# Optimization experiments

Measured on AMD Instinct MI355X. Metric: run time of the kernel, lower is better.

## Reference

```python
import jax, jax.numpy as jnp
import numpy as np

N, E = 20000, 5000
IN_FT, OUT_FT = 128, 128
DENSITY = 0.01  # fraction of nonzeros in the incidence matrix


def setup_inputs() -> dict:
    key = jax.random.key(0)
    kx, kh, kw, kb = jax.random.split(key, 4)
    X = jax.random.normal(kx, (N, IN_FT), dtype=jnp.float32)
    H = (jax.random.uniform(kh, (N, E)) < DENSITY).astype(jnp.float32)
    # xavier_normal_ with gain=0.01
    xav_std = 0.01 * np.sqrt(2.0 / (IN_FT + OUT_FT))
    weight_trans = jax.random.normal(kw, (IN_FT, OUT_FT), dtype=jnp.float32) * xav_std
    bias = jax.random.normal(kb, (OUT_FT,), dtype=jnp.float32) * 0.01
    return {"X": X, "H": H, "weight_trans": weight_trans, "bias": bias}


def reference(X, H, weight_trans, bias):
    # X: [N, in_ft], H: [N, E] incidence
    Xw = X @ weight_trans                      # [N, out_ft]
    DV = jnp.sum(H, axis=1) + 1e-12            # node degrees, [N]
    DE = jnp.sum(H, axis=0) + 1e-12            # hyperedge degrees, [E]
    # G = diag(1/DV) @ H @ diag(1/DE) @ H^T applied to Xw, computed in the
    # efficient order without materializing the NxN matrix G:
    M = H.T @ Xw                               # [E, out_ft]
    M = M / DE[:, None]                        # diag(1/DE) scaling
    out = H @ M                                # [N, out_ft]
    out = out / DV[:, None]                    # diag(1/DV) scaling
    out = out + bias
    return jax.nn.relu(out)
```

## Files before the change

### kernel.cpp

```cpp
#include <hip/hip_runtime.h>
#include <hip/hip_bf16.h>

typedef unsigned long long u64;
typedef unsigned int u32;
typedef unsigned short u16;
typedef __attribute__((ext_vector_type(4))) float f32x4v;
typedef __attribute__((ext_vector_type(16))) float f32x16;
typedef __attribute__((ext_vector_type(8))) short bf16x8;

#define N_NODES 20000
#define N_EDGES 5000
#define FT 128
#define NT 20
#define NRG 313
#define ROW_U64 80
#define COL_STRIDE 5120
#define XWT_S 20032

#define NTLOAD(p) __builtin_nontemporal_load((const f32x4v*)(p))

static __device__ __forceinline__ u64 spread4(u64 x) {
  x = (x | (x << 24)) & 0x000000FF000000FFull;
  x = (x | (x << 12)) & 0x000F000F000F000Full;
  x = (x | (x << 6))  & 0x0303030303030303ull;
  x = (x | (x << 3))  & 0x1111111111111111ull;
  return x;
}

static __device__ __forceinline__ u16 f2bf(float x) {
  u32 u = __float_as_uint(x);
  u = (u + 0x7FFFu + ((u >> 16) & 1u)) >> 16;
  return (u16)u;
}

static __device__ __forceinline__ bf16x8 expand8(u32 b) {
  union { u32 u[4]; bf16x8 v; } r;
  r.u[0] = (( b        & 1u) | ((( b >> 1) & 1u) << 16)) * 0x3F80u;
  r.u[1] = (((b >> 2)  & 1u) | ((( b >> 3) & 1u) << 16)) * 0x3F80u;
  r.u[2] = (((b >> 4)  & 1u) | ((( b >> 5) & 1u) << 16)) * 0x3F80u;
  r.u[3] = (((b >> 6)  & 1u) | ((( b >> 7) & 1u) << 16)) * 0x3F80u;
  return r.v;
}

static __device__ __forceinline__ int swz(int c, int r) {
  return c * 256 + (((r + c) & 31) << 3);
}

__global__ __launch_bounds__(256) void scan_fused(
    const float* __restrict__ H, u64* __restrict__ Hbt2, u64* __restrict__ HbtT,
    const float2* __restrict__ X2, __hip_bfloat162* __restrict__ Xb2,
    const float* __restrict__ Wf, u16* __restrict__ WtB) {
  const int wid = threadIdx.x >> 6, lane = threadIdx.x & 63;

  if (blockIdx.x >= 1565) {
    for (int i = (blockIdx.x - 1565) * 256 + threadIdx.x; i < 1280000;
         i += 320 * 256)
      Xb2[i] = __float22bfloat162_rn(X2[i]);
    if (blockIdx.x == 1884) {
      for (int i = threadIdx.x; i < FT * FT; i += 256) {
        int f = i >> 7, k = i & 127;
        WtB[i] = f2bf(Wf[k * FT + f]);
      }
    }
    return;
  }

  const int gw = blockIdx.x * 4 + wid;
  const int t = gw % NT, rg = gw / NT;
  const int r0 = rg * 64;
  const int rows = min(64, N_NODES - r0);
  const int idx4 = t * 64 + lane;
  const bool lv = idx4 < 1250;

  u64 m0 = 0, m1 = 0, m2 = 0, m3 = 0;
  for (int kb = 0; kb < rows; kb += 8) {
    f32x4v vv[8];
#pragma unroll
    for (int k = 0; k < 8; ++k) vv[k] = (f32x4v){0.f, 0.f, 0.f, 0.f};
    if (lv) {
      const float* bp = H + (size_t)(r0 + kb) * N_EDGES + idx4 * 4;
#pragma unroll
      for (int k = 0; k < 8; ++k) vv[k] = NTLOAD(bp + (size_t)k * N_EDGES);
    }
#pragma unroll
    for (int k = 0; k < 8; ++k) {
      u64 b0 = __ballot(vv[k].x != 0.f);
      u64 b1 = __ballot(vv[k].y != 0.f);
      u64 b2 = __ballot(vv[k].z != 0.f);
      u64 b3 = __ballot(vv[k].w != 0.f);
      const bool keep = (lane == kb + k);
      m0 = keep ? b0 : m0;  m1 = keep ? b1 : m1;
      m2 = keep ? b2 : m2;  m3 = keep ? b3 : m3;
    }
  }
  if (lane < rows) {
#pragma unroll
    for (int j = 0; j < 4; ++j) {
      u64 p = spread4((m0 >> (16 * j)) & 0xFFFFull)
            | (spread4((m1 >> (16 * j)) & 0xFFFFull) << 1)
            | (spread4((m2 >> (16 * j)) & 0xFFFFull) << 2)
            | (spread4((m3 >> (16 * j)) & 0xFFFFull) << 3);
      Hbt2[(size_t)(t * 4 + j) * N_NODES + (r0 + lane)] = p;
    }
  }
  u64 t0 = 0, t1 = 0, t2 = 0, t3 = 0;
  for (int l = 0; l < 64; ++l) {
    u64 c0 = __ballot((m0 >> l) & 1ull);
    u64 c1 = __ballot((m1 >> l) & 1ull);
    u64 c2 = __ballot((m2 >> l) & 1ull);
    u64 c3 = __ballot((m3 >> l) & 1ull);
    const bool keep = (lane == l);
    t0 = keep ? c0 : t0;  t1 = keep ? c1 : t1;
    t2 = keep ? c2 : t2;  t3 = keep ? c3 : t3;
  }
  u64* op = HbtT + (size_t)rg * COL_STRIDE + t * 256 + 4 * lane;
  op[0] = t0; op[1] = t1; op[2] = t2; op[3] = t3;
}

__global__ __launch_bounds__(256) void gemm_xw(
    const u16* __restrict__ Xb, const u16* __restrict__ WtB,
    u16* __restrict__ XwT) {
  __shared__ u16 xt[4096];
  const int wave = threadIdx.x >> 6, lane = threadIdx.x & 63;
  const int col = lane & 31, half = lane >> 5;
  const int n0 = blockIdx.x * 32;
  const int f0 = wave * 32;
  if (n0 >= N_NODES) {
    if (lane < 32)
      for (int r = 0; r < 32; ++r)
        XwT[(size_t)(f0 + r) * XWT_S + n0 + lane] = 0;
    return;
  }
  {
    const int sn = threadIdx.x >> 3, sc = threadIdx.x & 7;
#pragma unroll
    for (int j = 0; j < 2; ++j) {
      bf16x8 v = *(const bf16x8*)(Xb + (size_t)(n0 + sn) * FT + (sc + 8 * j) * 8);
      *(bf16x8*)(xt + sn * 128 + (((sc + 8 * j) + sn) & 15) * 8) = v;
    }
  }
  __syncthreads();
  f32x16 acc;
#pragma unroll
  for (int i = 0; i < 16; ++i) acc[i] = 0.f;
#pragma unroll
  for (int kc = 0; kc < 16; kc += 2) {
    int c = kc + half;
    bf16x8 a = *(const bf16x8*)(WtB + (f0 + col) * FT + c * 8);
    bf16x8 b = *(const bf16x8*)(xt + col * 128 + ((c + col) & 15) * 8);
    acc = __builtin_amdgcn_mfma_f32_32x32x16_bf16(a, b, acc, 0, 0, 0);
  }
#pragma unroll
  for (int r = 0; r < 16; ++r) {
    int fr = (r & 3) + 8 * (r >> 2) + 4 * half;
    XwT[(size_t)(f0 + fr) * XWT_S + n0 + col] = f2bf(acc[r]);
  }
}

__global__ __launch_bounds__(256) void edge_gemm(
    const u16* __restrict__ XwT, const u64* __restrict__ HbtT,
    u16* __restrict__ MhT) {
  __shared__ u16 atile[4][2][2048];
  __shared__ float sdv[4][32];
  const int tid = threadIdx.x;
  const int wid = tid >> 6, lane = tid & 63;
  const int col = lane & 31, half = lane >> 5;

  const int et = blockIdx.x % 160, ft = blockIdx.x / 160;
  const int e0 = et * 32, f0 = ft * 32;
  const int ws_ = wid * 78 + (wid > 0 ? 1 : 0);
  const int we_ = ws_ + (wid == 0 ? 79 : 78);

  const int srow = lane >> 3, schunk = lane & 7;
  const u16* sgbase = XwT + (size_t)(f0 + srow) * XWT_S + schunk * 8;
  u16* buf0 = &atile[wid][0][0];
  u16* buf1 = &atile[wid][1][0];

  f32x16 acc;
#pragma unroll
  for (int i = 0; i < 16; ++i) acc[i] = 0.f;
  float dv = 0.f;

  bf16x8 rB[4], rC[4];
  {
    const int w1 = (ws_ + 1 < we_) ? ws_ + 1 : ws_;
    bf16x8 rA[4];
#pragma unroll
    for (int j = 0; j < 4; ++j)
      rA[j] = *(const bf16x8*)(sgbase + (size_t)(8 * j) * XWT_S + ws_ * 64);
#pragma unroll
    for (int j = 0; j < 4; ++j)
      rB[j] = *(const bf16x8*)(sgbase + (size_t)(8 * j) * XWT_S + w1 * 64);
#pragma unroll
    for (int j = 0; j < 4; ++j)
      *(bf16x8*)(buf0 + swz(schunk, srow + 8 * j)) = rA[j];
  }
  u64 h0 = HbtT[(size_t)ws_ * COL_STRIDE + e0 + col];
  u64 h1 = HbtT[(size_t)((ws_ + 1 < we_) ? ws_ + 1 : ws_) * COL_STRIDE + e0 + col];

  int p = 0;
  for (int w = ws_; w < we_; ++w) {
    const int w2 = (w + 2 < we_) ? w + 2 : we_ - 1;
#pragma unroll
    for (int j = 0; j < 4; ++j)
      rC[j] = *(const bf16x8*)(sgbase + (size_t)(8 * j) * XWT_S + w2 * 64);
    u64 h2 = HbtT[(size_t)w2 * COL_STRIDE + e0 + col];

    const u16* ab = p ? buf1 : buf0;
#pragma unroll
    for (int q = 0; q < 4; ++q) {
      bf16x8 a = *(const bf16x8*)(ab + swz(2 * q + half, col));
      bf16x8 b = expand8((u32)(h0 >> (q * 16 + half * 8)) & 0xFFu);
      acc = __builtin_amdgcn_mfma_f32_32x32x16_bf16(a, b, acc, 0, 0, 0);
    }
    dv += (float)__popcll(h0);

    u16* nb = p ? buf0 : buf1;
#pragma unroll
    for (int j = 0; j < 4; ++j)
      *(bf16x8*)(nb + swz(schunk, srow + 8 * j)) = rB[j];
#pragma unroll
    for (int j = 0; j < 4; ++j) rB[j] = rC[j];
    h0 = h1; h1 = h2; p ^= 1;
  }

  float* sacc = (float*)&atile[wid][0][0];
#pragma unroll
  for (int r = 0; r < 16; ++r) {
    int fr = (r & 3) + 8 * (r >> 2) + 4 * half;
    sacc[fr * 32 + col] = acc[r];
  }
  if (half == 0) sdv[wid][col] = dv;
  __syncthreads();

  {
    const int frl = tid >> 3, eq = tid & 7;
    const float* s0 = (const float*)&atile[0][0][0];
    union { u16 h[4]; u64 q; } o;
#pragma unroll
    for (int j = 0; j < 4; ++j) {
      int e = eq * 4 + j;
      int idx = frl * 32 + e;
      float s = s0[idx] + s0[2048 + idx] + s0[4096 + idx] + s0[6144 + idx];
      float d = sdv[0][e] + sdv[1][e] + sdv[2][e] + sdv[3][e];
      o.h[j] = f2bf(s / (d + 1e-12f));
    }
    *(u64*)(MhT + (size_t)(f0 + frl) * COL_STRIDE + e0 + eq * 4) = o.q;
  }
}

__global__ __launch_bounds__(256) void node_gemm(
    const u64* __restrict__ Hbt2, const u16* __restrict__ MhT,
    const float* __restrict__ bias, float* __restrict__ out) {
  __shared__ u16 btile[4][2][2048];
  const int tid = threadIdx.x;
  const int wid = tid >> 6, lane = tid & 63;
  const int col = lane & 31, half = lane >> 5;
  const int n0 = blockIdx.x * 32;
  const int f0 = wid * 32;

  const int srow = lane >> 3, schunk = lane & 7;
  const u16* sgbase = MhT + (size_t)(f0 + srow) * COL_STRIDE + schunk * 8;
  u16* buf0 = &btile[wid][0][0];
  u16* buf1 = &btile[wid][1][0];

  f32x16 acc;
#pragma unroll
  for (int i = 0; i < 16; ++i) acc[i] = 0.f;
  float dv = 0.f;

  bf16x8 rB[4], rC[4];
  {
    bf16x8 rA[4];
#pragma unroll
    for (int j = 0; j < 4; ++j)
      rA[j] = *(const bf16x8*)(sgbase + (size_t)(8 * j) * COL_STRIDE);
#pragma unroll
    for (int j = 0; j < 4; ++j)
      rB[j] = *(const bf16x8*)(sgbase + (size_t)(8 * j) * COL_STRIDE + 64);
#pragma unroll
    for (int j = 0; j < 4; ++j)
      *(bf16x8*)(buf0 + swz(schunk, srow + 8 * j)) = rA[j];
  }
  u64 h0 = Hbt2[(size_t)0 * N_NODES + n0 + col];
  u64 h1 = Hbt2[(size_t)1 * N_NODES + n0 + col];

  int p = 0;
  for (int w = 0; w < ROW_U64; ++w) {
    const int w2 = (w + 2 < ROW_U64) ? w + 2 : ROW_U64 - 1;
#pragma unroll
    for (int j = 0; j < 4; ++j)
      rC[j] = *(const bf16x8*)(sgbase + (size_t)(8 * j) * COL_STRIDE + w2 * 64);
    u64 h2 = Hbt2[(size_t)w2 * N_NODES + n0 + col];

    const u16* bb = p ? buf1 : buf0;
#pragma unroll
    for (int q = 0; q < 4; ++q) {
      bf16x8 a = expand8((u32)(h0 >> (q * 16 + half * 8)) & 0xFFu);
      bf16x8 b = *(const bf16x8*)(bb + swz(2 * q + half, col));
      acc = __builtin_amdgcn_mfma_f32_32x32x16_bf16(a, b, acc, 0, 0, 0);
    }
    dv += (float)__popcll(h0);

    u16* nb = p ? buf0 : buf1;
#pragma unroll
    for (int j = 0; j < 4; ++j)
      *(bf16x8*)(nb + swz(schunk, srow + 8 * j)) = rB[j];
#pragma unroll
    for (int j = 0; j < 4; ++j) rB[j] = rC[j];
    h0 = h1; h1 = h2; p ^= 1;
  }

  float inv = 1.f / (dv + 1e-12f);
  float bb = bias[f0 + col];
#pragma unroll
  for (int r = 0; r < 16; ++r) {
    int rr = (r & 3) + 8 * (r >> 2) + 4 * half;
    float iv = __shfl(inv, rr);
    out[(size_t)(n0 + rr) * FT + f0 + col] = fmaxf(fmaf(acc[r], iv, bb), 0.f);
  }
}

extern "C" void kernel_launch(void* const* d_in, const int* in_sizes, int n_in,
                              void* d_out, int out_size, void* d_ws, size_t ws_size,
                              hipStream_t stream) {
  const float* X    = (const float*)d_in[0];
  const float* H    = (const float*)d_in[1];
  const float* W    = (const float*)d_in[2];
  const float* bias = (const float*)d_in[3];
  float* out = (float*)d_out;

  int* ws = (int*)d_ws;
  u64* Hbt2            = (u64*)ws;
  u64* HbtT            = (u64*)(ws + 3200000);
  __hip_bfloat162* Xb2 = (__hip_bfloat162*)(ws + 6405120);
  u16* MhT             = (u16*)(ws + 6405120);
  u16* WtB             = (u16*)(ws + 7685120);
  u16* XwT             = (u16*)(ws + 7693312);

  scan_fused<<<1885, 256, 0, stream>>>(H, Hbt2, HbtT, (const float2*)X, Xb2,
                                       W, WtB);
  gemm_xw   <<<626, 256, 0, stream>>>((const u16*)Xb2, WtB, XwT);
  edge_gemm <<<640, 256, 0, stream>>>(XwT, HbtT, MhT);
  node_gemm <<<625, 256, 0, stream>>>(Hbt2, MhT, bias, out);
}
```

Measured before the change: 653.5 us.

## Fuse four stage kernels into one persistent kernel with grid barriers

Merges the scan, Xw GEMM, edge GEMM and node GEMM kernels into a single persistent kernel of 768 blocks that loops over virtual block indices. Stages are separated by atomic-counter grid barriers, and shared memory is held in a union sized for the largest stage. The aim is to remove three kernel launches and the gaps between them. In exchange it adds a memset launch, spin-wait barriers that rely on every block being co-resident, and a fixed grid that may leave work unevenly spread across CUs within each stage.

```diff
diff --git a/kernel.cpp b/kernel.cpp
--- a/kernel.cpp
+++ b/kernel.cpp
@@ -16,6 +16,7 @@
 #define ROW_U64 80
 #define COL_STRIDE 5120
 #define XWT_S 20032
+#define GRID 768
 
 #define NTLOAD(p) __builtin_nontemporal_load((const f32x4v*)(p))
 
@@ -46,287 +47,303 @@
   return c * 256 + (((r + c) & 31) << 3);
 }
 
-__global__ __launch_bounds__(256) void scan_fused(
+static __device__ __forceinline__ void gbar(int* bar, int target) {
+  __syncthreads();
+  if (threadIdx.x == 0) {
+    __threadfence();
+    atomicAdd(bar, 1);
+    int spins = 0;
+    while (__hip_atomic_load(bar, __ATOMIC_RELAXED,
+                             __HIP_MEMORY_SCOPE_AGENT) < target) {
+      __builtin_amdgcn_s_sleep(4);
+      if (++spins > (1 << 26)) break;
+    }
+    __threadfence();
+  }
+  __syncthreads();
+}
+
+union SharedU {
+  struct { u16 xt[4096]; } x;
+  struct { u16 atile[4][2][2048]; float sdv[4][32]; } e;
+  struct { u16 btile[4][2][2048]; } n;
+};
+
+__global__ __launch_bounds__(256, 3) void mega(
     const float* __restrict__ H, u64* __restrict__ Hbt2, u64* __restrict__ HbtT,
     const float2* __restrict__ X2, __hip_bfloat162* __restrict__ Xb2,
-    const float* __restrict__ Wf, u16* __restrict__ WtB) {
-  const int wid = threadIdx.x >> 6, lane = threadIdx.x & 63;
-
-  if (blockIdx.x >= 1565) {
-    for (int i = (blockIdx.x - 1565) * 256 + threadIdx.x; i < 1280000;
-         i += 320 * 256)
-      Xb2[i] = __float22bfloat162_rn(X2[i]);
-    if (blockIdx.x == 1884) {
-      for (int i = threadIdx.x; i < FT * FT; i += 256) {
-        int f = i >> 7, k = i & 127;
-        WtB[i] = f2bf(Wf[k * FT + f]);
-      }
-    }
-    return;
-  }
-
-  const int gw = blockIdx.x * 4 + wid;
-  const int t = gw % NT, rg = gw / NT;
-  const int r0 = rg * 64;
-  const int rows = min(64, N_NODES - r0);
-  const int idx4 = t * 64 + lane;
-  const bool lv = idx4 < 1250;
-
-  u64 m0 = 0, m1 = 0, m2 = 0, m3 = 0;
-  for (int kb = 0; kb < rows; kb += 8) {
-    f32x4v vv[8];
-#pragma unroll
-    for (int k = 0; k < 8; ++k) vv[k] = (f32x4v){0.f, 0.f, 0.f, 0.f};
-    if (lv) {
-      const float* bp = H + (size_t)(r0 + kb) * N_EDGES + idx4 * 4;
-#pragma unroll
-      for (int k = 0; k < 8; ++k) vv[k] = NTLOAD(bp + (size_t)k * N_EDGES);
-    }
-#pragma unroll
-    for (int k = 0; k < 8; ++k) {
-      u64 b0 = __ballot(vv[k].x != 0.f);
-      u64 b1 = __ballot(vv[k].y != 0.f);
-      u64 b2 = __ballot(vv[k].z != 0.f);
-      u64 b3 = __ballot(vv[k].w != 0.f);
-      const bool keep = (lane == kb + k);
-      m0 = keep ? b0 : m0;  m1 = keep ? b1 : m1;
-      m2 = keep ? b2 : m2;  m3 = keep ? b3 : m3;
-    }
-  }
-  if (lane < rows) {
-#pragma unroll
-    for (int j = 0; j < 4; ++j) {
-      u64 p = spread4((m0 >> (16 * j)) & 0xFFFFull)
-            | (spread4((m1 >> (16 * j)) & 0xFFFFull) << 1)
-            | (spread4((m2 >> (16 * j)) & 0xFFFFull) << 2)
-            | (spread4((m3 >> (16 * j)) & 0xFFFFull) << 3);
-      Hbt2[(size_t)(t * 4 + j) * N_NODES + (r0 + lane)] = p;
-    }
-  }
-  u64 t0 = 0, t1 = 0, t2 = 0, t3 = 0;
-  for (int l = 0; l < 64; ++l) {
-    u64 c0 = __ballot((m0 >> l) & 1ull);
-    u64 c1 = __ballot((m1 >> l) & 1ull);
-    u64 c2 = __ballot((m2 >> l) & 1ull);
-    u64 c3 = __ballot((m3 >> l) & 1ull);
-    const bool keep = (lane == l);
-    t0 = keep ? c0 : t0;  t1 = keep ? c1 : t1;
-    t2 = keep ? c2 : t2;  t3 = keep ? c3 : t3;
-  }
-  u64* op = HbtT + (size_t)rg * COL_STRIDE + t * 256 + 4 * lane;
-  op[0] = t0; op[1] = t1; op[2] = t2; op[3] = t3;
-}
-
-__global__ __launch_bounds__(256) void gemm_xw(
-    const u16* __restrict__ Xb, const u16* __restrict__ WtB,
-    u16* __restrict__ XwT) {
-  __shared__ u16 xt[4096];
-  const int wave = threadIdx.x >> 6, lane = threadIdx.x & 63;
-  const int col = lane & 31, half = lane >> 5;
-  const int n0 = blockIdx.x * 32;
-  const int f0 = wave * 32;
-  if (n0 >= N_NODES) {
-    if (lane < 32)
-      for (int r = 0; r < 32; ++r)
-        XwT[(size_t)(f0 + r) * XWT_S + n0 + lane] = 0;
-    return;
-  }
-  {
-    const int sn = threadIdx.x >> 3, sc = threadIdx.x & 7;
-#pragma unroll
-    for (int j = 0; j < 2; ++j) {
-      bf16x8 v = *(const bf16x8*)(Xb + (size_t)(n0 + sn) * FT + (sc + 8 * j) * 8);
-      *(bf16x8*)(xt + sn * 128 + (((sc + 8 * j) + sn) & 15) * 8) = v;
-    }
-  }
-  __syncthreads();
-  f32x16 acc;
-#pragma unroll
-  for (int i = 0; i < 16; ++i) acc[i] = 0.f;
-#pragma unroll
-  for (int kc = 0; kc < 16; kc += 2) {
-    int c = kc + half;
-    bf16x8 a = *(const bf16x8*)(WtB + (f0 + col) * FT + c * 8);
-    bf16x8 b = *(const bf16x8*)(xt + col * 128 + ((c + col) & 15) * 8);
-    acc = __builtin_amdgcn_mfma_f32_32x32x16_bf16(a, b, acc, 0, 0, 0);
-  }
-#pragma unroll
-  for (int r = 0; r < 16; ++r) {
-    int fr = (r & 3) + 8 * (r >> 2) + 4 * half;
-    XwT[(size_t)(f0 + fr) * XWT_S + n0 + col] = f2bf(acc[r]);
-  }
-}
-
-__global__ __launch_bounds__(256) void edge_gemm(
-    const u16* __restrict__ XwT, const u64* __restrict__ HbtT,
-    u16* __restrict__ MhT) {
-  __shared__ u16 atile[4][2][2048];
-  __shared__ float sdv[4][32];
+    const float* __restrict__ Wf, u16* __restrict__ WtB,
+    u16* __restrict__ XwT, u16* __restrict__ MhT,
+    const float* __restrict__ bias, float* __restrict__ out,
+    int* __restrict__ bar) {
+  __shared__ SharedU sh;
   const int tid = threadIdx.x;
   const int wid = tid >> 6, lane = tid & 63;
   const int col = lane & 31, half = lane >> 5;
 
-  const int et = blockIdx.x % 160, ft = blockIdx.x / 160;
-  const int e0 = et * 32, f0 = ft * 32;
-  const int ws_ = wid * 78 + (wid > 0 ? 1 : 0);
-  const int we_ = ws_ + (wid == 0 ? 79 : 78);
-
-  const int srow = lane >> 3, schunk = lane & 7;
-  const u16* sgbase = XwT + (size_t)(f0 + srow) * XWT_S + schunk * 8;
-  u16* buf0 = &atile[wid][0][0];
-  u16* buf1 = &atile[wid][1][0];
-
-  f32x16 acc;
-#pragma unroll
-  for (int i = 0; i < 16; ++i) acc[i] = 0.f;
-  float dv = 0.f;
-
-  bf16x8 rB[4], rC[4];
-  {
-    const int w1 = (ws_ + 1 < we_) ? ws_ + 1 : ws_;
-    bf16x8 rA[4];
-#pragma unroll
-    for (int j = 0; j < 4; ++j)
-      rA[j] = *(const bf16x8*)(sgbase + (size_t)(8 * j) * XWT_S + ws_ * 64);
-#pragma unroll
-    for (int j = 0; j < 4; ++j)
-      rB[j] = *(const bf16x8*)(sgbase + (size_t)(8 * j) * XWT_S + w1 * 64);
-#pragma unroll
-    for (int j = 0; j < 4; ++j)
-      *(bf16x8*)(buf0 + swz(schunk, srow + 8 * j)) = rA[j];
-  }
-  u64 h0 = HbtT[(size_t)ws_ * COL_STRIDE + e0 + col];
-  u64 h1 = HbtT[(size_t)((ws_ + 1 < we_) ? ws_ + 1 : ws_) * COL_STRIDE + e0 + col];
-
-  int p = 0;
-  for (int w = ws_; w < we_; ++w) {
-    const int w2 = (w + 2 < we_) ? w + 2 : we_ - 1;
-#pragma unroll
-    for (int j = 0; j < 4; ++j)
-      rC[j] = *(const bf16x8*)(sgbase + (size_t)(8 * j) * XWT_S + w2 * 64);
-    u64 h2 = HbtT[(size_t)w2 * COL_STRIDE + e0 + col];
-
-    const u16* ab = p ? buf1 : buf0;
-#pragma unroll
-    for (int q = 0; q < 4; ++q) {
-      bf16x8 a = *(const bf16x8*)(ab + swz(2 * q + half, col));
-      bf16x8 b = expand8((u32)(h0 >> (q * 16 + half * 8)) & 0xFFu);
-      acc = __builtin_amdgcn_mfma_f32_32x32x16_bf16(a, b, acc, 0, 0, 0);
-    }
-    dv += (float)__popcll(h0);
-
-    u16* nb = p ? buf0 : buf1;
-#pragma unroll
-    for (int j = 0; j < 4; ++j)
-      *(bf16x8*)(nb + swz(schunk, srow + 8 * j)) = rB[j];
-#pragma unroll
-    for (int j = 0; j < 4; ++j) rB[j] = rC[j];
-    h0 = h1; h1 = h2; p ^= 1;
-  }
-
-  float* sacc = (float*)&atile[wid][0][0];
-#pragma unroll
-  for (int r = 0; r < 16; ++r) {
-    int fr = (r & 3) + 8 * (r >> 2) + 4 * half;
-    sacc[fr * 32 + col] = acc[r];
-  }
-  if (half == 0) sdv[wid][col] = dv;
-  __syncthreads();
-
-  {
-    const int frl = tid >> 3, eq = tid & 7;
-    const float* s0 = (const float*)&atile[0][0][0];
-    union { u16 h[4]; u64 q; } o;
-#pragma unroll
-    for (int j = 0; j < 4; ++j) {
-      int e = eq * 4 + j;
-      int idx = frl * 32 + e;
-      float s = s0[idx] + s0[2048 + idx] + s0[4096 + idx] + s0[6144 + idx];
-      float d = sdv[0][e] + sdv[1][e] + sdv[2][e] + sdv[3][e];
-      o.h[j] = f2bf(s / (d + 1e-12f));
-    }
-    *(u64*)(MhT + (size_t)(f0 + frl) * COL_STRIDE + e0 + eq * 4) = o.q;
-  }
-}
-
-__global__ __launch_bounds__(256) void node_gemm(
-    const u64* __restrict__ Hbt2, const u16* __restrict__ MhT,
-    const float* __restrict__ bias, float* __restrict__ out) {
-  __shared__ u16 btile[4][2][2048];
-  const int tid = threadIdx.x;
-  const int wid = tid >> 6, lane = tid & 63;
-  const int col = lane & 31, half = lane >> 5;
-  const int n0 = blockIdx.x * 32;
-  const int f0 = wid * 32;
-
-  const int srow = lane >> 3, schunk = lane & 7;
-  const u16* sgbase = MhT + (size_t)(f0 + srow) * COL_STRIDE + schunk * 8;
-  u16* buf0 = &btile[wid][0][0];
-  u16* buf1 = &btile[wid][1][0];
-
-  f32x16 acc;
-#pragma unroll
-  for (int i = 0; i < 16; ++i) acc[i] = 0.f;
-  float dv = 0.f;
-
-  bf16x8 rB[4], rC[4];
-  {
-    bf16x8 rA[4];
-#pragma unroll
-    for (int j = 0; j < 4; ++j)
-      rA[j] = *(const bf16x8*)(sgbase + (size_t)(8 * j) * COL_STRIDE);
-#pragma unroll
-    for (int j = 0; j < 4; ++j)
-      rB[j] = *(const bf16x8*)(sgbase + (size_t)(8 * j) * COL_STRIDE + 64);
-#pragma unroll
-    for (int j = 0; j < 4; ++j)
-      *(bf16x8*)(buf0 + swz(schunk, srow + 8 * j)) = rA[j];
-  }
-  u64 h0 = Hbt2[(size_t)0 * N_NODES + n0 + col];
-  u64 h1 = Hbt2[(size_t)1 * N_NODES + n0 + col];
-
-  int p = 0;
-  for (int w = 0; w < ROW_U64; ++w) {
-    const int w2 = (w + 2 < ROW_U64) ? w + 2 : ROW_U64 - 1;
-#pragma unroll
-    for (int j = 0; j < 4; ++j)
-      rC[j] = *(const bf16x8*)(sgbase + (size_t)(8 * j) * COL_STRIDE + w2 * 64);
-    u64 h2 = Hbt2[(size_t)w2 * N_NODES + n0 + col];
-
-    const u16* bb = p ? buf1 : buf0;
-#pragma unroll
-    for (int q = 0; q < 4; ++q) {
-      bf16x8 a = expand8((u32)(h0 >> (q * 16 + half * 8)) & 0xFFu);
-      bf16x8 b = *(const bf16x8*)(bb + swz(2 * q + half, col));
-      acc = __builtin_amdgcn_mfma_f32_32x32x16_bf16(a, b, acc, 0, 0, 0);
-    }
-    dv += (float)__popcll(h0);
-
-    u16* nb = p ? buf0 : buf1;
-#pragma unroll
-    for (int j = 0; j < 4; ++j)
-      *(bf16x8*)(nb + swz(schunk, srow + 8 * j)) = rB[j];
-#pragma unroll
-    for (int j = 0; j < 4; ++j) rB[j] = rC[j];
-    h0 = h1; h1 = h2; p ^= 1;
-  }
-
-  float inv = 1.f / (dv + 1e-12f);
-  float bb = bias[f0 + col];
-#pragma unroll
-  for (int r = 0; r < 16; ++r) {
-    int rr = (r & 3) + 8 * (r >> 2) + 4 * half;
-    float iv = __shfl(inv, rr);
-    out[(size_t)(n0 + rr) * FT + f0 + col] = fmaxf(fmaf(acc[r], iv, bb), 0.f);
+  for (int vb = blockIdx.x; vb < 1885; vb += GRID) {
+    if (vb >= 1565) {
+      for (int i = (vb - 1565) * 256 + tid; i < 1280000; i += 320 * 256)
+        Xb2[i] = __float22bfloat162_rn(X2[i]);
+      if (vb == 1884) {
+        for (int i = tid; i < FT * FT; i += 256) {
+          int f = i >> 7, k = i & 127;
+          WtB[i] = f2bf(Wf[k * FT + f]);
+        }
+      }
+      continue;
+    }
+    const int gw = vb * 4 + wid;
+    const int t = gw % NT, rg = gw / NT;
+    const int r0 = rg * 64;
+    const int rows = min(64, N_NODES - r0);
+    const int idx4 = t * 64 + lane;
+    const bool lv = idx4 < 1250;
+
+    u64 m0 = 0, m1 = 0, m2 = 0, m3 = 0;
+    for (int kb = 0; kb < rows; kb += 8) {
+      f32x4v vv[8];
+#pragma unroll
+      for (int k = 0; k < 8; ++k) vv[k] = (f32x4v){0.f, 0.f, 0.f, 0.f};
+      if (lv) {
+        const float* bp = H + (size_t)(r0 + kb) * N_EDGES + idx4 * 4;
+#pragma unroll
+        for (int k = 0; k < 8; ++k) vv[k] = NTLOAD(bp + (size_t)k * N_EDGES);
+      }
+#pragma unroll
+      for (int k = 0; k < 8; ++k) {
+        u64 b0 = __ballot(vv[k].x != 0.f);
+        u64 b1 = __ballot(vv[k].y != 0.f);
+        u64 b2 = __ballot(vv[k].z != 0.f);
+        u64 b3 = __ballot(vv[k].w != 0.f);
+        const bool keep = (lane == kb + k);
+        m0 = keep ? b0 : m0;  m1 = keep ? b1 : m1;
+        m2 = keep ? b2 : m2;  m3 = keep ? b3 : m3;
+      }
+    }
+    if (lane < rows) {
+#pragma unroll
+      for (int j = 0; j < 4; ++j) {
+        u64 p = spread4((m0 >> (16 * j)) & 0xFFFFull)
+              | (spread4((m1 >> (16 * j)) & 0xFFFFull) << 1)
+              | (spread4((m2 >> (16 * j)) & 0xFFFFull) << 2)
+              | (spread4((m3 >> (16 * j)) & 0xFFFFull) << 3);
+        Hbt2[(size_t)(t * 4 + j) * N_NODES + (r0 + lane)] = p;
+      }
+    }
+    u64 t0 = 0, t1 = 0, t2 = 0, t3 = 0;
+    for (int l = 0; l < 64; ++l) {
+      u64 c0 = __ballot((m0 >> l) & 1ull);
+      u64 c1 = __ballot((m1 >> l) & 1ull);
+      u64 c2 = __ballot((m2 >> l) & 1ull);
+      u64 c3 = __ballot((m3 >> l) & 1ull);
+      const bool keep = (lane == l);
+      t0 = keep ? c0 : t0;  t1 = keep ? c1 : t1;
+      t2 = keep ? c2 : t2;  t3 = keep ? c3 : t3;
+    }
+    u64* op = HbtT + (size_t)rg * COL_STRIDE + t * 256 + 4 * lane;
+    op[0] = t0; op[1] = t1; op[2] = t2; op[3] = t3;
+  }
+  gbar(bar, GRID);
+
+  for (int vb = blockIdx.x; vb < 626; vb += GRID) {
+    const int n0 = vb * 32;
+    const int f0 = wid * 32;
+    if (n0 >= N_NODES) {
+      if (lane < 32)
+        for (int r = 0; r < 32; ++r)
+          XwT[(size_t)(f0 + r) * XWT_S + n0 + lane] = 0;
+    } else {
+      __syncthreads();
+      const u16* Xb = (const u16*)Xb2;
+      {
+        const int sn = tid >> 3, sc = tid & 7;
+#pragma unroll
+        for (int j = 0; j < 2; ++j) {
+          bf16x8 v = *(const bf16x8*)(Xb + (size_t)(n0 + sn) * FT + (sc + 8 * j) * 8);
+          *(bf16x8*)(sh.x.xt + sn * 128 + (((sc + 8 * j) + sn) & 15) * 8) = v;
+        }
+      }
+      __syncthreads();
+      f32x16 acc;
+#pragma unroll
+      for (int i = 0; i < 16; ++i) acc[i] = 0.f;
+#pragma unroll
+      for (int kc = 0; kc < 16; kc += 2) {
+        int c = kc + half;
+        bf16x8 a = *(const bf16x8*)(WtB + (f0 + col) * FT + c * 8);
+        bf16x8 b = *(const bf16x8*)(sh.x.xt + col * 128 + ((c + col) & 15) * 8);
+        acc = __builtin_amdgcn_mfma_f32_32x32x16_bf16(a, b, acc, 0, 0, 0);
+      }
+#pragma unroll
+      for (int r = 0; r < 16; ++r) {
+        int fr = (r & 3) + 8 * (r >> 2) + 4 * half;
+        XwT[(size_t)(f0 + fr) * XWT_S + n0 + col] = f2bf(acc[r]);
+      }
+    }
+  }
+  gbar(bar, 2 * GRID);
+
+  for (int vb = blockIdx.x; vb < 640; vb += GRID) {
+    const int et = vb % 160, ft = vb / 160;
+    const int e0 = et * 32, f0 = ft * 32;
+    const int ws_ = wid * 78 + (wid > 0 ? 1 : 0);
+    const int we_ = ws_ + (wid == 0 ? 79 : 78);
+
+    const int srow = lane >> 3, schunk = lane & 7;
+    const u16* sgbase = XwT + (size_t)(f0 + srow) * XWT_S + schunk * 8;
+    u16* buf0 = &sh.e.atile[wid][0][0];
+    u16* buf1 = &sh.e.atile[wid][1][0];
+
+    __syncthreads();
+
+    f32x16 acc;
+#pragma unroll
+    for (int i = 0; i < 16; ++i) acc[i] = 0.f;
+    float dv = 0.f;
+
+    bf16x8 rB[4], rC[4];
+    {
+      const int w1 = (ws_ + 1 < we_) ? ws_ + 1 : ws_;
+      bf16x8 rA[4];
+#pragma unroll
+      for (int j = 0; j < 4; ++j)
+        rA[j] = *(const bf16x8*)(sgbase + (size_t)(8 * j) * XWT_S + ws_ * 64);
+#pragma unroll
+      for (int j = 0; j < 4; ++j)
+        rB[j] = *(const bf16x8*)(sgbase + (size_t)(8 * j) * XWT_S + w1 * 64);
+#pragma unroll
+      for (int j = 0; j < 4; ++j)
+        *(bf16x8*)(buf0 + swz(schunk, srow + 8 * j)) = rA[j];
+    }
+    u64 h0 = HbtT[(size_t)ws_ * COL_STRIDE + e0 + col];
+    u64 h1 = HbtT[(size_t)((ws_ + 1 < we_) ? ws_ + 1 : ws_) * COL_STRIDE + e0 + col];
+
+    int p = 0;
+    for (int w = ws_; w < we_; ++w) {
+      const int w2 = (w + 2 < we_) ? w + 2 : we_ - 1;
+#pragma unroll
+      for (int j = 0; j < 4; ++j)
+        rC[j] = *(const bf16x8*)(sgbase + (size_t)(8 * j) * XWT_S + w2 * 64);
+      u64 h2 = HbtT[(size_t)w2 * COL_STRIDE + e0 + col];
+
+      const u16* ab = p ? buf1 : buf0;
+#pragma unroll
+      for (int q = 0; q < 4; ++q) {
+        bf16x8 a = *(const bf16x8*)(ab + swz(2 * q + half, col));
+        bf16x8 b = expand8((u32)(h0 >> (q * 16 + half * 8)) & 0xFFu);
+        acc = __builtin_amdgcn_mfma_f32_32x32x16_bf16(a, b, acc, 0, 0, 0);
+      }
+      dv += (float)__popcll(h0);
+
+      u16* nb = p ? buf0 : buf1;
+#pragma unroll
+      for (int j = 0; j < 4; ++j)
+        *(bf16x8*)(nb + swz(schunk, srow + 8 * j)) = rB[j];
+#pragma unroll
+      for (int j = 0; j < 4; ++j) rB[j] = rC[j];
+      h0 = h1; h1 = h2; p ^= 1;
+    }
+
+    float* sacc = (float*)&sh.e.atile[wid][0][0];
+#pragma unroll
+    for (int r = 0; r < 16; ++r) {
+      int fr = (r & 3) + 8 * (r >> 2) + 4 * half;
+      sacc[fr * 32 + col] = acc[r];
+    }
+    if (half == 0) sh.e.sdv[wid][col] = dv;
+    __syncthreads();
+
+    {
+      const int frl = tid >> 3, eq = tid & 7;
+      const float* s0 = (const float*)&sh.e.atile[0][0][0];
+      union { u16 h[4]; u64 q; } o;
+#pragma unroll
+      for (int j = 0; j < 4; ++j) {
+        int e = eq * 4 + j;
+        int idx = frl * 32 + e;
+        float s = s0[idx] + s0[2048 + idx] + s0[4096 + idx] + s0[6144 + idx];
+        float d = sh.e.sdv[0][e] + sh.e.sdv[1][e] + sh.e.sdv[2][e] + sh.e.sdv[3][e];
+        o.h[j] = f2bf(s / (d + 1e-12f));
+      }
+      *(u64*)(MhT + (size_t)(f0 + frl) * COL_STRIDE + e0 + eq * 4) = o.q;
+    }
+  }
+  gbar(bar, 3 * GRID);
+
+  for (int vb = blockIdx.x; vb < 625; vb += GRID) {
+    const int n0 = vb * 32;
+    const int f0 = wid * 32;
+
+    const int srow = lane >> 3, schunk = lane & 7;
+    const u16* sgbase = MhT + (size_t)(f0 + srow) * COL_STRIDE + schunk * 8;
+    u16* buf0 = &sh.n.btile[wid][0][0];
+    u16* buf1 = &sh.n.btile[wid][1][0];
+
+    f32x16 acc;
+#pragma unroll
+    for (int i = 0; i < 16; ++i) acc[i] = 0.f;
+    float dv = 0.f;
+
+    bf16x8 rB[4], rC[4];
+    {
+      bf16x8 rA[4];
+#pragma unroll
+      for (int j = 0; j < 4; ++j)
+        rA[j] = *(const bf16x8*)(sgbase + (size_t)(8 * j) * COL_STRIDE);
+#pragma unroll
+      for (int j = 0; j < 4; ++j)
+        rB[j] = *(const bf16x8*)(sgbase + (size_t)(8 * j) * COL_STRIDE + 64);
+#pragma unroll
+      for (int j = 0; j < 4; ++j)
+        *(bf16x8*)(buf0 + swz(schunk, srow + 8 * j)) = rA[j];
+    }
+    u64 h0 = Hbt2[(size_t)0 * N_NODES + n0 + col];
+    u64 h1 = Hbt2[(size_t)1 * N_NODES + n0 + col];
+
+    int p = 0;
+    for (int w = 0; w < ROW_U64; ++w) {
+      const int w2 = (w + 2 < ROW_U64) ? w + 2 : ROW_U64 - 1;
+#pragma unroll
+      for (int j = 0; j < 4; ++j)
+        rC[j] = *(const bf16x8*)(sgbase + (size_t)(8 * j) * COL_STRIDE + w2 * 64);
+      u64 h2 = Hbt2[(size_t)w2 * N_NODES + n0 + col];
+
+      const u16* bb = p ? buf1 : buf0;
+#pragma unroll
+      for (int q = 0; q < 4; ++q) {
+        bf16x8 a = expand8((u32)(h0 >> (q * 16 + half * 8)) & 0xFFu);
+        bf16x8 b = *(const bf16x8*)(bb + swz(2 * q + half, col));
+        acc = __builtin_amdgcn_mfma_f32_32x32x16_bf16(a, b, acc, 0, 0, 0);
+      }
+      dv += (float)__popcll(h0);
+
+      u16* nb = p ? buf0 : buf1;
+#pragma unroll
+      for (int j = 0; j < 4; ++j)
+        *(bf16x8*)(nb + swz(schunk, srow + 8 * j)) = rB[j];
+#pragma unroll
+      for (int j = 0; j < 4; ++j) rB[j] = rC[j];
+      h0 = h1; h1 = h2; p ^= 1;
+    }
+
+    float inv = 1.f / (dv + 1e-12f);
+    float bb = bias[f0 + col];
+#pragma unroll
+    for (int r = 0; r < 16; ++r) {
+      int rr = (r & 3) + 8 * (r >> 2) + 4 * half;
+      float iv = __shfl(inv, rr);
+      out[(size_t)(n0 + rr) * FT + f0 + col] = fmaxf(fmaf(acc[r], iv, bb), 0.f);
+    }
   }
 }
 
 extern "C" void kernel_launch(void* const* d_in, const int* in_sizes, int n_in,
                               void* d_out, int out_size, void* d_ws, size_t ws_size,
                               hipStream_t stream) {
-  const float* X    = (const float*)d_in[0];
-  const float* H    = (const float*)d_in[1];
-  const float* W    = (const float*)d_in[2];
+  const float* Xf   = (const float*)d_in[0];
+  const float* Hf   = (const float*)d_in[1];
+  const float* Wf   = (const float*)d_in[2];
   const float* bias = (const float*)d_in[3];
   float* out = (float*)d_out;
 
@@ -337,10 +354,11 @@
   u16* MhT             = (u16*)(ws + 6405120);
   u16* WtB             = (u16*)(ws + 7685120);
   u16* XwT             = (u16*)(ws + 7693312);
-
-  scan_fused<<<1885, 256, 0, stream>>>(H, Hbt2, HbtT, (const float2*)X, Xb2,
-                                       W, WtB);
-  gemm_xw   <<<626, 256, 0, stream>>>((const u16*)Xb2, WtB, XwT);
-  edge_gemm <<<640, 256, 0, stream>>>(XwT, HbtT, MhT);
-  node_gemm <<<625, 256, 0, stream>>>(Hbt2, MhT, bias, out);
-}
+  int* bar             = ws + 8975360;
+
+  hipMemsetAsync(bar, 0, 64, stream);
+
+  const float2* X2 = (const float2*)Xf;
+  mega<<<GRID, 256, 0, stream>>>(Hf, Hbt2, HbtT, X2, Xb2, Wf, WtB,
+                                 XwT, MhT, bias, out, bar);
+}
```

Result: slower. 901.8 us (+38.0%).
